# Kernel tuning notes

Hardware: AMD Instinct MI355X
Metric: run time of the kernel (lower is better)

The kernel has to match this reference:

```python
import jax, jax.numpy as jnp
import numpy as np

GRAPH_WEIGHT = 10.0
SIGMA = 1.0
EPS = 1e-8


def setup_inputs() -> dict:
    key = jax.random.key(0)
    k1, k2, k3 = jax.random.split(key, 3)
    B, N, BS, K = 2, 16384, 128, 8
    NB = N // BS
    Nsup, Nig = N // 4, N // 8
    logits = jax.random.normal(k1, (B, N, 1), dtype=jnp.float32)
    targets_sup = jax.random.uniform(k2, (B, Nsup), dtype=jnp.float32)  # soft labels in [0,1)
    pos = jax.random.uniform(k3, (B, N, 2), dtype=jnp.float32) * 10.0   # spatial coords
    idx = jnp.arange(N)
    sup_mask = jnp.broadcast_to(idx < Nsup, (B, N))
    ignore_mask = jnp.broadcast_to((idx >= Nsup) & (idx < Nsup + Nig), (B, N))
    # local window of K neighbor blocks per query block (clipped at edges)
    qb = jnp.arange(NB)
    win = jnp.arange(K) - K // 2
    kv_indices = jnp.broadcast_to(jnp.clip(qb[:, None] + win[None, :], 0, NB - 1), (B, NB, K)).astype(jnp.int32)
    kv_num_blocks = jnp.full((B, NB), K, dtype=jnp.int32)
    return {"logits": logits, "targets_sup": targets_sup, "pos": pos,
            "sup_mask": sup_mask, "ignore_mask": ignore_mask,
            "kv_indices": kv_indices, "kv_num_blocks": kv_num_blocks}


def _graph_smoothness(logits, pos, sup_mask, ignore_mask, kv_indices, kv_num_blocks):
    B, N, _ = logits.shape
    NB = kv_num_blocks.shape[1]
    BS = N // NB
    K = kv_indices.shape[2]
    probs = jax.nn.sigmoid(logits[..., 0])                      # [B,N]
    uncertain = (~ignore_mask) & (~sup_mask)                    # [B,N]

    off = jnp.arange(BS)
    q_nodes = jnp.arange(NB)[:, None] * BS + off[None, :]       # [NB,BS]
    nb_nodes = (kv_indices[..., None] * BS + off[None, None, None, :]).reshape(B, NB, K * BS)  # [B,NB,KBS]
    b_ar = jnp.arange(B)[:, None, None]

    q_probs = probs[:, q_nodes]                                 # [B,NB,BS]
    q_pos = pos[:, q_nodes, :2]                                 # [B,NB,BS,2]
    q_valid = uncertain[:, q_nodes]                             # [B,NB,BS]

    k_probs = probs[b_ar, nb_nodes]                             # [B,NB,KBS]
    k_pos = pos[b_ar, nb_nodes][..., :2]                        # [B,NB,KBS,2]
    block_valid = jnp.arange(K)[None, None, :] < kv_num_blocks[:, :, None]  # [B,NB,K]
    k_valid = (~ignore_mask[b_ar, nb_nodes]) & jnp.repeat(block_valid, BS, axis=2)  # [B,NB,KBS]

    # pairwise euclidean distances via |q|^2 + |k|^2 - 2 q.k (avoids [.,.,2] broadcast blowup)
    qn2 = jnp.sum(q_pos * q_pos, axis=-1)                       # [B,NB,BS]
    kn2 = jnp.sum(k_pos * k_pos, axis=-1)                       # [B,NB,KBS]
    d2 = qn2[..., :, None] + kn2[..., None, :] - 2.0 * jnp.einsum('bqid,bqjd->bqij', q_pos, k_pos)
    dists = jnp.sqrt(jnp.maximum(d2, 0.0))                      # [B,NB,BS,KBS]

    is_self = q_nodes[None, :, :, None] == nb_nodes[:, :, None, :]
    weights = jnp.exp(-dists / SIGMA)
    weights = jnp.where(is_self | (~k_valid[:, :, None, :]), 0.0, weights)
    wsum = jnp.sum(weights, axis=-1, keepdims=True)
    weights = weights / (wsum + EPS)
    k_mean = jnp.einsum('bqij,bqj->bqi', weights, k_probs)      # [B,NB,BS]

    block_has_k = jnp.any(k_valid, axis=-1)                     # [B,NB]
    count_mask = q_valid & block_has_k[:, :, None]              # [B,NB,BS]
    sq = jnp.where(count_mask, (q_probs - k_mean) ** 2, 0.0)
    loss_b = jnp.sum(sq, axis=(1, 2))                           # [B]
    num_q = jnp.sum(count_mask, axis=(1, 2))                    # [B] int
    valid = num_q > 0
    per_batch = jnp.where(valid, loss_b / jnp.maximum(num_q, 1).astype(loss_b.dtype), 0.0)
    n_valid = jnp.maximum(jnp.sum(valid.astype(jnp.int32)), 1)
    return jnp.sum(per_batch) / n_valid.astype(per_batch.dtype)


def reference(logits, targets_sup, pos, sup_mask, ignore_mask, kv_indices, kv_num_blocks):
    # supervised BCE on the first Nsup nodes of each batch (== logits[sup_mask])
    Nsup = targets_sup.shape[1]
    ls = logits[:, :Nsup, 0]
    bce = jnp.maximum(ls, 0.0) - ls * targets_sup + jnp.log1p(jnp.exp(-jnp.abs(ls)))
    loss_sup = jnp.mean(bce)
    loss_graph = _graph_smoothness(logits, pos, sup_mask, ignore_mask, kv_indices, kv_num_blocks)
    return loss_sup + GRAPH_WEIGHT * loss_graph
```

## Files before the change

kernel.cpp:

```cpp
#include <hip/hip_runtime.h>
#include <math.h>

#define BB   2
#define NN   16384
#define BS   128
#define KW   8
#define NB   128
#define NSUP 4096
#define NIG  2048
#define NEI  1024
#define EPSF 1e-8f
#define GW   10.0f
#define LOG2E 1.4426950408889634f
#define LN2   0.6931471805599453f

#define QB0    48
#define NQB    (NB - QB0)
#define QPB    8
#define GRAPH_BLOCKS (BB * NQB * 16)
#define UNITS_PER_B  (NQB * 16)
#define BCE_BLOCKS 32

__device__ __forceinline__ float fexp2(float x) { return __builtin_amdgcn_exp2f(x); }
__device__ __forceinline__ float fsqrt(float x) { return __builtin_amdgcn_sqrtf(x); }
__device__ __forceinline__ float frcp (float x) { return __builtin_amdgcn_rcpf(x); }
__device__ __forceinline__ float flog2(float x) { return __builtin_amdgcn_logf(x); }
__device__ __forceinline__ float fsigmoid(float x) { return frcp(1.0f + fexp2(-x * LOG2E)); }

__global__ __launch_bounds__(256, 8) void graph_kernel(
    const float* __restrict__ logits,
    const float* __restrict__ targets,
    const float* __restrict__ pos,
    const int*   __restrict__ kv_indices,
    const int*   __restrict__ kv_num_blocks,
    float* __restrict__ part_loss,
    float* __restrict__ part_cnt,
    float* __restrict__ part_bce)
{
    __shared__ float4 s_n[NEI];
    __shared__ float4 s_q[QPB];
    __shared__ int    s_info;
    __shared__ float  s_redl[4];
    __shared__ float  s_redb[4];

    const int bid   = blockIdx.x;
    const int b     = bid / UNITS_PER_B;
    const int r     = bid - b * UNITS_PER_B;
    const int qb    = QB0 + (r >> 4);
    const int piece = r & 15;
    const int tid   = threadIdx.x;
    const int bq    = b * NB + qb;
    const int knb   = kv_num_blocks[bq];

    if (tid == 0) {
        int cs = 0, has = 0;
        for (int k = 0; k < knb; ++k) {
            const int blk = kv_indices[bq * KW + k];
            cs += (blk == qb);
            const int lo = blk * BS;
            has |= !(lo >= NSUP && lo + BS <= NSUP + NIG);
        }
        s_info = (has ? 1 : 0) | (cs << 8);
    }

    #pragma unroll
    for (int t = 0; t < 4; ++t) {
        const int i    = t * 256 + tid;
        const int k    = i >> 7;
        const int blk  = kv_indices[bq * KW + k];
        const int node = blk * BS + (i & (BS - 1));
        const size_t gi = (size_t)b * NN + node;
        const float p   = fsigmoid(logits[gi]);
        const float2 xy = ((const float2*)pos)[gi];
        const bool valid = (k < knb) && !(node >= NSUP && node < NSUP + NIG);
        s_n[i] = make_float4(valid ? xy.x * LOG2E : 1e19f,
                             valid ? xy.y * LOG2E : 0.0f, p, 0.0f);
    }
    if (tid < QPB) {
        const int qidx = qb * BS + piece * QPB + tid;
        const size_t gi = (size_t)b * NN + qidx;
        const float2 xy = ((const float2*)pos)[gi];
        s_q[tid] = make_float4(xy.x * LOG2E, xy.y * LOG2E, fsigmoid(logits[gi]), 0.0f);
    }
    __syncthreads();

    const int c = tid & 63;
    const int g = tid >> 6;

    float qx[2], qy[2], qp[2], a[4];
    #pragma unroll
    for (int qq = 0; qq < 2; ++qq) {
        const float4 qv = s_q[g * 2 + qq];
        qx[qq] = qv.x; qy[qq] = qv.y; qp[qq] = qv.z;
        a[qq] = 0.0f; a[2 + qq] = 0.0f;
    }

    #pragma unroll 4
    for (int t = 0; t < NEI / 64; ++t) {
        const float4 nb = s_n[t * 64 + c];
        #pragma unroll
        for (int qq = 0; qq < 2; ++qq) {
            const float dx = qx[qq] - nb.x;
            const float dy = qy[qq] - nb.y;
            const float d  = fsqrt(__builtin_fmaf(dx, dx, dy * dy));
            const float w  = fexp2(-d);
            a[qq]     += w;
            a[2 + qq]  = __builtin_fmaf(w, nb.z, a[2 + qq]);
        }
    }

    {
        const bool up0 = (tid & 1) != 0;
        #pragma unroll
        for (int i = 0; i < 2; ++i) {
            const float keep = up0 ? a[i + 2] : a[i];
            const float send = up0 ? a[i] : a[i + 2];
            a[i] = keep + __shfl_xor(send, 1);
        }
        const bool up1 = (tid & 2) != 0;
        const float keep = up1 ? a[1] : a[0];
        const float send = up1 ? a[0] : a[1];
        a[0] = keep + __shfl_xor(send, 2);
    }
    a[0] += __shfl_xor(a[0], 4);
    a[0] += __shfl_xor(a[0], 8);
    a[0] += __shfl_xor(a[0], 16);
    a[0] += __shfl_xor(a[0], 32);
    const float wp_o = __shfl_xor(a[0], 1);

    const int info = s_info;
    float sq = 0.0f;
    if ((c & 1) == 0 && c < 4) {
        const int qq = c >> 1;
        const float cself = (float)(info >> 8);
        const float qpv   = s_q[g * 2 + qq].z;
        const float wsf   = a[0] - cself;
        const float wpf   = wp_o - cself * qpv;
        const float km    = wpf * frcp(wsf + EPSF);
        const float df    = qpv - km;
        sq = (info & 1) ? df * df : 0.0f;
    }
    sq += __shfl_xor(sq, 2);
    if (c == 0) s_redl[g] = sq;

    float bsum = 0.0f;
    if (bid < BCE_BLOCKS) {
        const int e  = bid * 256 + tid;
        const int bb = e >> 12;
        const int ii = e & 4095;
        const float ls = logits[(size_t)bb * NN + ii];
        const float tt = targets[e];
        float bce = fmaxf(ls, 0.0f) - ls * tt
                  + flog2(1.0f + fexp2(-fabsf(ls) * LOG2E)) * LN2;
        #pragma unroll
        for (int off = 1; off < 64; off <<= 1) bce += __shfl_xor(bce, off);
        bsum = bce;
    }
    if (c == 0) s_redb[g] = bsum;
    __syncthreads();

    if (tid == 0) {
        part_loss[bid] = (s_redl[0] + s_redl[1]) + (s_redl[2] + s_redl[3]);
        part_cnt[bid]  = (info & 1) ? (float)QPB : 0.0f;
        if (bid < BCE_BLOCKS)
            part_bce[bid] = (s_redb[0] + s_redb[1]) + (s_redb[2] + s_redb[3]);
    }
}

__global__ __launch_bounds__(256) void final_kernel(
    const float* __restrict__ part_loss,
    const float* __restrict__ part_cnt,
    const float* __restrict__ part_bce,
    float* __restrict__ out)
{
    __shared__ float s_fr[5][4];
    const int tid = threadIdx.x;

    float l0 = 0.0f, l1 = 0.0f, c0 = 0.0f, c1 = 0.0f, bc = 0.0f;
    #pragma unroll
    for (int j = tid; j < UNITS_PER_B; j += 256) {
        l0 += part_loss[j];
        l1 += part_loss[UNITS_PER_B + j];
        c0 += part_cnt[j];
        c1 += part_cnt[UNITS_PER_B + j];
    }
    if (tid < BCE_BLOCKS) bc = part_bce[tid];

    #pragma unroll
    for (int off = 1; off < 64; off <<= 1) {
        l0 += __shfl_xor(l0, off);  l1 += __shfl_xor(l1, off);
        c0 += __shfl_xor(c0, off);  c1 += __shfl_xor(c1, off);
        bc += __shfl_xor(bc, off);
    }
    const int wave = tid >> 6, lane = tid & 63;
    if (lane == 0) {
        s_fr[0][wave] = l0; s_fr[1][wave] = l1;
        s_fr[2][wave] = c0; s_fr[3][wave] = c1; s_fr[4][wave] = bc;
    }
    __syncthreads();
    if (tid == 0) {
        float L0 = 0, L1 = 0, C0 = 0, C1 = 0, Bc = 0;
        #pragma unroll
        for (int w = 0; w < 4; ++w) {
            L0 += s_fr[0][w]; L1 += s_fr[1][w];
            C0 += s_fr[2][w]; C1 += s_fr[3][w]; Bc += s_fr[4][w];
        }
        const float loss_sup = Bc / (float)(BB * NSUP);
        float total = 0.0f; int nv = 0;
        if (C0 > 0.0f) { total += L0 / C0; nv++; }
        if (C1 > 0.0f) { total += L1 / C1; nv++; }
        out[0] = loss_sup + GW * (total / (float)(nv > 0 ? nv : 1));
    }
}

extern "C" void kernel_launch(void* const* d_in, const int* in_sizes, int n_in,
                              void* d_out, int out_size, void* d_ws, size_t ws_size,
                              hipStream_t stream) {
    const float* logits        = (const float*)d_in[0];
    const float* targets_sup   = (const float*)d_in[1];
    const float* pos           = (const float*)d_in[2];
    const int*   kv_indices    = (const int*)d_in[5];
    const int*   kv_num_blocks = (const int*)d_in[6];
    float* out = (float*)d_out;

    float* part_loss = (float*)d_ws;
    float* part_cnt  = (float*)((char*)d_ws + (size_t)2560 * 4);
    float* part_bce  = (float*)((char*)d_ws + (size_t)5120 * 4);

    graph_kernel<<<GRAPH_BLOCKS, 256, 0, stream>>>(
        logits, targets_sup, pos, kv_indices, kv_num_blocks,
        part_loss, part_cnt, part_bce);
    final_kernel<<<1, 256, 0, stream>>>(part_loss, part_cnt, part_bce, out);
}
```

Measured before the change: 17.70 us.

## Split graph loss into prep, chunked pairwise, and two-stage reduction kernels

```diff
diff --git a/kernel.cpp b/kernel.cpp
--- a/kernel.cpp
+++ b/kernel.cpp
@@ -8,18 +8,20 @@
 #define NB   128
 #define NSUP 4096
 #define NIG  2048
-#define NEI  1024
 #define EPSF 1e-8f
 #define GW   10.0f
 #define LOG2E 1.4426950408889634f
 #define LN2   0.6931471805599453f
 
-#define QB0    48
-#define NQB    (NB - QB0)
-#define QPB    8
-#define GRAPH_BLOCKS (BB * NQB * 16)
-#define UNITS_PER_B  (NQB * 16)
-#define BCE_BLOCKS 32
+#define QB0  48
+#define NQB  80
+#define QTOT (BB * NQB * BS)
+#define NCH  16
+#define B_BLOCKS (BB * NQB * NCH)
+#define PREP_BLOCKS 128
+#define C1_BLOCKS (BB * NQB)
+#define IGB0 (NSUP / BS)
+#define IGB1 ((NSUP + NIG) / BS)
 
 __device__ __forceinline__ float fexp2(float x) { return __builtin_amdgcn_exp2f(x); }
 __device__ __forceinline__ float fsqrt(float x) { return __builtin_amdgcn_sqrtf(x); }
@@ -27,164 +29,146 @@
 __device__ __forceinline__ float flog2(float x) { return __builtin_amdgcn_logf(x); }
 __device__ __forceinline__ float fsigmoid(float x) { return frcp(1.0f + fexp2(-x * LOG2E)); }
 
-__global__ __launch_bounds__(256, 8) void graph_kernel(
+__global__ __launch_bounds__(256) void prep_kernel(
     const float* __restrict__ logits,
     const float* __restrict__ targets,
     const float* __restrict__ pos,
-    const int*   __restrict__ kv_indices,
-    const int*   __restrict__ kv_num_blocks,
-    float* __restrict__ part_loss,
-    float* __restrict__ part_cnt,
+    float4* __restrict__ nodes,
     float* __restrict__ part_bce)
 {
-    __shared__ float4 s_n[NEI];
-    __shared__ float4 s_q[QPB];
-    __shared__ int    s_info;
-    __shared__ float  s_redl[4];
-    __shared__ float  s_redb[4];
-
-    const int bid   = blockIdx.x;
-    const int b     = bid / UNITS_PER_B;
-    const int r     = bid - b * UNITS_PER_B;
-    const int qb    = QB0 + (r >> 4);
-    const int piece = r & 15;
-    const int tid   = threadIdx.x;
-    const int bq    = b * NB + qb;
-    const int knb   = kv_num_blocks[bq];
-
-    if (tid == 0) {
-        int cs = 0, has = 0;
-        for (int k = 0; k < knb; ++k) {
-            const int blk = kv_indices[bq * KW + k];
-            cs += (blk == qb);
-            const int lo = blk * BS;
-            has |= !(lo >= NSUP && lo + BS <= NSUP + NIG);
-        }
-        s_info = (has ? 1 : 0) | (cs << 8);
-    }
-
-    #pragma unroll
-    for (int t = 0; t < 4; ++t) {
-        const int i    = t * 256 + tid;
-        const int k    = i >> 7;
-        const int blk  = kv_indices[bq * KW + k];
-        const int node = blk * BS + (i & (BS - 1));
-        const size_t gi = (size_t)b * NN + node;
-        const float p   = fsigmoid(logits[gi]);
-        const float2 xy = ((const float2*)pos)[gi];
-        const bool valid = (k < knb) && !(node >= NSUP && node < NSUP + NIG);
-        s_n[i] = make_float4(valid ? xy.x * LOG2E : 1e19f,
-                             valid ? xy.y * LOG2E : 0.0f, p, 0.0f);
-    }
-    if (tid < QPB) {
-        const int qidx = qb * BS + piece * QPB + tid;
-        const size_t gi = (size_t)b * NN + qidx;
-        const float2 xy = ((const float2*)pos)[gi];
-        s_q[tid] = make_float4(xy.x * LOG2E, xy.y * LOG2E, fsigmoid(logits[gi]), 0.0f);
-    }
+    const int bid = blockIdx.x, tid = threadIdx.x;
+    const int b = bid >> 6;
+    const int n = ((bid & 63) << 8) + tid;
+    const size_t gi = (size_t)b * NN + n;
+    const float lg = logits[gi];
+    const float2 xy = ((const float2*)pos)[gi];
+    nodes[gi] = make_float4(xy.x * LOG2E, xy.y * LOG2E, fsigmoid(lg), 0.0f);
+
+    float bce = 0.0f;
+    if (n < NSUP) {
+        const float tt = targets[(size_t)b * NSUP + n];
+        bce = fmaxf(lg, 0.0f) - lg * tt
+            + flog2(1.0f + fexp2(-fabsf(lg) * LOG2E)) * LN2;
+    }
+    #pragma unroll
+    for (int off = 1; off < 64; off <<= 1) bce += __shfl_xor(bce, off);
+    __shared__ float s[4];
+    if ((tid & 63) == 0) s[tid >> 6] = bce;
     __syncthreads();
-
-    const int c = tid & 63;
-    const int g = tid >> 6;
-
-    float qx[2], qy[2], qp[2], a[4];
-    #pragma unroll
-    for (int qq = 0; qq < 2; ++qq) {
-        const float4 qv = s_q[g * 2 + qq];
-        qx[qq] = qv.x; qy[qq] = qv.y; qp[qq] = qv.z;
-        a[qq] = 0.0f; a[2 + qq] = 0.0f;
-    }
-
-    #pragma unroll 4
-    for (int t = 0; t < NEI / 64; ++t) {
-        const float4 nb = s_n[t * 64 + c];
-        #pragma unroll
-        for (int qq = 0; qq < 2; ++qq) {
-            const float dx = qx[qq] - nb.x;
-            const float dy = qy[qq] - nb.y;
+    if (tid == 0) part_bce[bid] = (s[0] + s[1]) + (s[2] + s[3]);
+}
+
+__global__ __launch_bounds__(128) void graph_kernel(
+    const float4* __restrict__ nodes,
+    const int*    __restrict__ kv_indices,
+    const int*    __restrict__ kv_num_blocks,
+    float2* __restrict__ part)
+{
+    const int bid = blockIdx.x;
+    const int ch  = bid & (NCH - 1);
+    const int u   = bid >> 4;
+    const int b   = (u >= NQB) ? 1 : 0;
+    const int qbr = u - b * NQB;
+    const int qb  = QB0 + qbr;
+    const int bq  = b * NB + qb;
+    const int tid = threadIdx.x;
+    const int lane = tid & 63, half = tid >> 6;
+
+    const int k    = ch >> 1;
+    const int joff = (ch & 1) << 6;
+
+    int knb = kv_num_blocks[bq];
+    int blk = kv_indices[bq * KW + k];
+    knb = __builtin_amdgcn_readfirstlane(knb);
+    blk = __builtin_amdgcn_readfirstlane(blk);
+
+    float ws = 0.0f, wp = 0.0f;
+    const bool active = (k < knb) && !(blk >= IGB0 && blk < IGB1);
+    if (active) {
+        const int qidx = qb * BS + half * 64 + lane;
+        const float4 qv = nodes[(size_t)b * NN + qidx];
+        const float4* __restrict__ nbp = nodes + ((size_t)b * NN + blk * BS + joff);
+        #pragma unroll 8
+        for (int j = 0; j < 64; ++j) {
+            const float4 nv = nbp[j];
+            const float dx = qv.x - nv.x;
+            const float dy = qv.y - nv.y;
             const float d  = fsqrt(__builtin_fmaf(dx, dx, dy * dy));
             const float w  = fexp2(-d);
-            a[qq]     += w;
-            a[2 + qq]  = __builtin_fmaf(w, nb.z, a[2 + qq]);
+            ws += w;
+            wp = __builtin_fmaf(w, nv.z, wp);
         }
     }
-
-    {
-        const bool up0 = (tid & 1) != 0;
-        #pragma unroll
-        for (int i = 0; i < 2; ++i) {
-            const float keep = up0 ? a[i + 2] : a[i];
-            const float send = up0 ? a[i] : a[i + 2];
-            a[i] = keep + __shfl_xor(send, 1);
+    part[(size_t)ch * QTOT + u * BS + tid] = make_float2(ws, wp);
+}
+
+__global__ __launch_bounds__(128) void c1_kernel(
+    const float4* __restrict__ nodes,
+    const int*    __restrict__ kv_indices,
+    const int*    __restrict__ kv_num_blocks,
+    const float2* __restrict__ part,
+    float* __restrict__ qb_loss,
+    float* __restrict__ qb_cnt)
+{
+    const int bid = blockIdx.x;
+    const int b   = (bid >= NQB) ? 1 : 0;
+    const int qbr = bid - b * NQB;
+    const int qb  = QB0 + qbr;
+    const int bq  = b * NB + qb;
+    const int tid = threadIdx.x;
+
+    const int knb = kv_num_blocks[bq];
+    int cself = 0, has = 0;
+    #pragma unroll
+    for (int k = 0; k < KW; ++k) {
+        if (k < knb) {
+            const int blk = kv_indices[bq * KW + k];
+            cself += (blk == qb);
+            has |= !(blk >= IGB0 && blk < IGB1);
         }
-        const bool up1 = (tid & 2) != 0;
-        const float keep = up1 ? a[1] : a[0];
-        const float send = up1 ? a[0] : a[1];
-        a[0] = keep + __shfl_xor(send, 2);
-    }
-    a[0] += __shfl_xor(a[0], 4);
-    a[0] += __shfl_xor(a[0], 8);
-    a[0] += __shfl_xor(a[0], 16);
-    a[0] += __shfl_xor(a[0], 32);
-    const float wp_o = __shfl_xor(a[0], 1);
-
-    const int info = s_info;
-    float sq = 0.0f;
-    if ((c & 1) == 0 && c < 4) {
-        const int qq = c >> 1;
-        const float cself = (float)(info >> 8);
-        const float qpv   = s_q[g * 2 + qq].z;
-        const float wsf   = a[0] - cself;
-        const float wpf   = wp_o - cself * qpv;
-        const float km    = wpf * frcp(wsf + EPSF);
-        const float df    = qpv - km;
-        sq = (info & 1) ? df * df : 0.0f;
-    }
-    sq += __shfl_xor(sq, 2);
-    if (c == 0) s_redl[g] = sq;
-
-    float bsum = 0.0f;
-    if (bid < BCE_BLOCKS) {
-        const int e  = bid * 256 + tid;
-        const int bb = e >> 12;
-        const int ii = e & 4095;
-        const float ls = logits[(size_t)bb * NN + ii];
-        const float tt = targets[e];
-        float bce = fmaxf(ls, 0.0f) - ls * tt
-                  + flog2(1.0f + fexp2(-fabsf(ls) * LOG2E)) * LN2;
-        #pragma unroll
-        for (int off = 1; off < 64; off <<= 1) bce += __shfl_xor(bce, off);
-        bsum = bce;
-    }
-    if (c == 0) s_redb[g] = bsum;
+    }
+
+    float ws = 0.0f, wp = 0.0f;
+    #pragma unroll
+    for (int c2 = 0; c2 < NCH; ++c2) {
+        const float2 v = part[(size_t)c2 * QTOT + bid * BS + tid];
+        ws += v.x; wp += v.y;
+    }
+    const int qidx = qb * BS + tid;
+    const float qp = nodes[(size_t)b * NN + qidx].z;
+    const float cs = (float)cself;
+    ws -= cs;
+    wp -= cs * qp;
+    const float km = wp * frcp(ws + EPSF);
+    const float df = qp - km;
+    float sq = has ? df * df : 0.0f;
+
+    #pragma unroll
+    for (int off = 1; off < 64; off <<= 1) sq += __shfl_xor(sq, off);
+    __shared__ float s[2];
+    if ((tid & 63) == 0) s[tid >> 6] = sq;
     __syncthreads();
-
     if (tid == 0) {
-        part_loss[bid] = (s_redl[0] + s_redl[1]) + (s_redl[2] + s_redl[3]);
-        part_cnt[bid]  = (info & 1) ? (float)QPB : 0.0f;
-        if (bid < BCE_BLOCKS)
-            part_bce[bid] = (s_redb[0] + s_redb[1]) + (s_redb[2] + s_redb[3]);
-    }
-}
-
-__global__ __launch_bounds__(256) void final_kernel(
-    const float* __restrict__ part_loss,
-    const float* __restrict__ part_cnt,
+        qb_loss[bid] = s[0] + s[1];
+        qb_cnt[bid]  = has ? (float)BS : 0.0f;
+    }
+}
+
+__global__ __launch_bounds__(256) void c2_kernel(
+    const float* __restrict__ qb_loss,
+    const float* __restrict__ qb_cnt,
     const float* __restrict__ part_bce,
     float* __restrict__ out)
 {
     __shared__ float s_fr[5][4];
     const int tid = threadIdx.x;
 
-    float l0 = 0.0f, l1 = 0.0f, c0 = 0.0f, c1 = 0.0f, bc = 0.0f;
-    #pragma unroll
-    for (int j = tid; j < UNITS_PER_B; j += 256) {
-        l0 += part_loss[j];
-        l1 += part_loss[UNITS_PER_B + j];
-        c0 += part_cnt[j];
-        c1 += part_cnt[UNITS_PER_B + j];
-    }
-    if (tid < BCE_BLOCKS) bc = part_bce[tid];
+    float l0 = 0, l1 = 0, c0 = 0, c1 = 0, bc = 0;
+    if (tid < NQB) {
+        l0 = qb_loss[tid];        c0 = qb_cnt[tid];
+        l1 = qb_loss[NQB + tid];  c1 = qb_cnt[NQB + tid];
+    }
+    if (tid < PREP_BLOCKS) bc = part_bce[tid];
 
     #pragma unroll
     for (int off = 1; off < 64; off <<= 1) {
@@ -223,12 +207,16 @@
     const int*   kv_num_blocks = (const int*)d_in[6];
     float* out = (float*)d_out;
 
-    float* part_loss = (float*)d_ws;
-    float* part_cnt  = (float*)((char*)d_ws + (size_t)2560 * 4);
-    float* part_bce  = (float*)((char*)d_ws + (size_t)5120 * 4);
-
-    graph_kernel<<<GRAPH_BLOCKS, 256, 0, stream>>>(
-        logits, targets_sup, pos, kv_indices, kv_num_blocks,
-        part_loss, part_cnt, part_bce);
-    final_kernel<<<1, 256, 0, stream>>>(part_loss, part_cnt, part_bce, out);
-}
+    char* w = (char*)d_ws;
+    float2* part     = (float2*)w;
+    size_t off = (size_t)NCH * QTOT * sizeof(float2);
+    float4* nodes    = (float4*)(w + off);  off += (size_t)BB * NN * sizeof(float4);
+    float*  part_bce = (float*)(w + off);   off += PREP_BLOCKS * sizeof(float);
+    float*  qb_loss  = (float*)(w + off);   off += C1_BLOCKS * sizeof(float);
+    float*  qb_cnt   = (float*)(w + off);
+
+    prep_kernel<<<PREP_BLOCKS, 256, 0, stream>>>(logits, targets_sup, pos, nodes, part_bce);
+    graph_kernel<<<B_BLOCKS, 128, 0, stream>>>(nodes, kv_indices, kv_num_blocks, part);
+    c1_kernel<<<C1_BLOCKS, 128, 0, stream>>>(nodes, kv_indices, kv_num_blocks, part, qb_loss, qb_cnt);
+    c2_kernel<<<1, 256, 0, stream>>>(qb_loss, qb_cnt, part_bce, out);
+}
```

After: 23.79 us. +34.4%, slower.
